# Kernel optimization log

Hardware: AMD Instinct MI355X
Metric: run time of the kernel (lower is better)

The kernel has to match this reference:

```python
import jax, jax.numpy as jnp
import numpy as np

NEG_INF = -9e15  # matches the source's -9000000000000000.0 mask fill
ALPHA = 0.2      # leaky_relu negative slope


def setup_inputs() -> dict:
    key = jax.random.key(0)
    k1, k2, k3, k4 = jax.random.split(key, 4)
    B, N, C_IN, C_OUT, H = 2, 2048, 128, 128, 16
    c = C_OUT // H  # 8 per-head features; equals H//2 so source's a-slice is consistent
    node_feats = jax.random.normal(k1, (B, N, C_IN), dtype=jnp.float32)
    # random 0/1 adjacency with self-loops
    adj = jax.random.randint(k2, (B, N, N), 0, 2).astype(jnp.float32)
    adj = jnp.maximum(adj, jnp.eye(N, dtype=jnp.float32)[None])
    # glorot-uniform-ish params
    W = jax.random.normal(k3, (C_IN, H * c), dtype=jnp.float32) * np.sqrt(2.0 / (C_IN + H * c))
    b = jnp.zeros((H * c,), dtype=jnp.float32)
    a = jax.random.normal(k4, (H, 2 * c), dtype=jnp.float32) * np.sqrt(2.0 / (H + 2 * c))
    return {"node_feats": node_feats, "adj_matrix": adj, "W": W, "b": b, "a": a}


def reference(node_feats, adj_matrix, W, b, a):
    B, N = node_feats.shape[:2]
    H = a.shape[0]
    c = a.shape[1] // 2
    # projection + split into heads: [B, N, H, c]
    h = (node_feats @ W + b).reshape(B, N, H, c)
    # additive attention halves (source slices a along last axis)
    logit_parent = jnp.einsum('bnhc,hc->bnh', h, a[:, :c])
    logit_child = jnp.einsum('bnhc,hc->bnh', h, a[:, c:])
    # dense broadcast-add logits: [B, N(i), N(j), H]
    attn_logits = logit_parent[:, :, None, :] + logit_child[:, None, :, :]
    attn_logits = jax.nn.leaky_relu(attn_logits, negative_slope=ALPHA)
    attn_logits = jnp.where(adj_matrix[..., None] == 1.0, attn_logits, NEG_INF)
    attn_probs = jax.nn.softmax(attn_logits, axis=2)  # over source nodes j
    out = jnp.einsum('bijh,bjhc->bihc', attn_probs, h)
    out = out.reshape(B, N, H * c)  # concat_heads=True
    return out, adj_matrix
```

## Files before the change

kernel.cpp:

```cpp
#include <hip/hip_runtime.h>
#include <hip/hip_bf16.h>


#define B_   2
#define N_   2048
#define CIN_ 128
#define H_   16

typedef _Float16 h2  __attribute__((ext_vector_type(2)));
typedef _Float16 v8h __attribute__((ext_vector_type(8)));
typedef float    v4f __attribute__((ext_vector_type(4)));

#define SC6 0.015625f

__device__ inline h2 pk_f16(float a, float b) {
  return __builtin_bit_cast(h2, __builtin_amdgcn_cvt_pkrtz(a, b));
}
__device__ inline unsigned as_u32(h2 v) { return __builtin_bit_cast(unsigned, v); }
__device__ inline h2 as_h2(unsigned u) { return __builtin_bit_cast(h2, u); }

__global__ __launch_bounds__(128) void proj_kernel(
    const float* __restrict__ nf, const float* __restrict__ W,
    const float* __restrict__ bias, const float* __restrict__ a,
    unsigned* __restrict__ hQ, unsigned* __restrict__ qI,
    float* __restrict__ lpT, unsigned* __restrict__ ones) {
  const int row0 = blockIdx.x * 4;
  const int t    = threadIdx.x;
  if (blockIdx.x == 0) {
    ones[t] = 0x3C003C00u; ones[t + 128] = 0x3C003C00u;
    ones[t + 256] = 0x3C003C00u; ones[t + 384] = 0x3C003C00u;
  }
  __shared__ float sNf[4][CIN_];
  ((float4*)&sNf[0][0])[t] = ((const float4*)(nf + (long)row0 * CIN_))[t];
  __syncthreads();
  float acc[4];
  const float bv = bias[t];
#pragma unroll
  for (int r = 0; r < 4; ++r) acc[r] = bv;
#pragma unroll 8
  for (int k = 0; k < CIN_; ++k) {
    const float w = W[k * 128 + t];
#pragma unroll
    for (int r = 0; r < 4; ++r) acc[r] = fmaf(sNf[r][k], w, acc[r]);
  }
  const int h = t >> 3, kc = t & 7;
  const int b = row0 >> 11, n0 = row0 & (N_ - 1);
  const int bh = b * H_ + h;
  const int cdw = n0 >> 1;
  uint2 hv;
  hv.x = as_u32(pk_f16(acc[0], acc[1]));
  hv.y = as_u32(pk_f16(acc[2], acc[3]));
  *(uint2*)(hQ + ((long)(bh * 8 + kc)) * (N_ / 2) + cdw) = hv;

  const float ap = a[h * 16 + kc], ac = a[h * 16 + 8 + kc];
  float lpv[4], lcv[4];
#pragma unroll
  for (int r = 0; r < 4; ++r) {
    float x = acc[r] * ap, y = acc[r] * ac;
#pragma unroll
    for (int s = 1; s < 8; s <<= 1) {
      x += __shfl_xor(x, s);
      y += __shfl_xor(y, s);
    }
    lpv[r] = x; lcv[r] = y;
  }
  if (kc == 0) {
    float4 l0 = {lpv[0], lpv[1], lpv[2], lpv[3]};
    *(float4*)(lpT + (long)bh * N_ + n0) = l0;
    uint2 q1, q2;
    q1.x = as_u32(pk_f16(__expf(lcv[0]) * SC6, __expf(lcv[1]) * SC6));
    q1.y = as_u32(pk_f16(__expf(lcv[2]) * SC6, __expf(lcv[3]) * SC6));
    q2.x = as_u32(pk_f16(__expf(0.2f * lcv[0]) * SC6, __expf(0.2f * lcv[1]) * SC6));
    q2.y = as_u32(pk_f16(__expf(0.2f * lcv[2]) * SC6, __expf(0.2f * lcv[3]) * SC6));
    const int addr = bh * 2048 + (cdw >> 4) * 32 + ((cdw >> 2) & 3) * 8;
    const int off  = cdw & 3;
    *(uint2*)(qI + addr + off)     = q1;
    *(uint2*)(qI + addr + 4 + off) = q2;
  }
}

__global__ __launch_bounds__(512) void attn_kernel(
    const float* __restrict__ adj, const unsigned* __restrict__ hQ,
    const unsigned* __restrict__ qI, const float* __restrict__ lpT,
    const unsigned* __restrict__ ones, float* __restrict__ pA,
    float* __restrict__ pL, float* __restrict__ adj_out) {
  const int jq   = blockIdx.x & 3;
  const int rest = blockIdx.x >> 2;
  const int b    = rest >> 6;
  const int i0   = (rest & 63) * 32;
  const int tid  = threadIdx.x;
  const int w    = tid >> 6;
  const int lane = tid & 63;

  __shared__ uint4 sA[2048];

  {
    const long aoff = (long)(b * N_ + i0) * N_ + jq * 512;
    const float* abase = adj + aoff;
    float* obase = adj_out + aoff;
    float4 fa[4], fb[4];
    int rowv[4], ccv[4];
#pragma unroll
    for (int s = 0; s < 4; ++s) {
      const int D = s * 512 + tid;
      const int u = D >> 10, loc = D & 1023;
      const int mm = loc & 15, qc = loc >> 4;
      ccv[s] = (qc >> 2) * 32 + (qc & 3) * 8;
      rowv[s] = u * 16 + mm;
      fa[s] = *(const float4*)(abase + (long)rowv[s] * N_ + ccv[s]);
      fb[s] = *(const float4*)(abase + (long)rowv[s] * N_ + ccv[s] + 4);
    }
#pragma unroll
    for (int s = 0; s < 4; ++s) {
      const int D = s * 512 + tid;
      uint4 uu;
      uu.x = as_u32(pk_f16(fa[s].x, fa[s].y)); uu.y = as_u32(pk_f16(fa[s].z, fa[s].w));
      uu.z = as_u32(pk_f16(fb[s].x, fb[s].y)); uu.w = as_u32(pk_f16(fb[s].z, fb[s].w));
      sA[D] = uu;
      *(float4*)(obase + (long)rowv[s] * N_ + ccv[s])     = fa[s];
      *(float4*)(obase + (long)rowv[s] * N_ + ccv[s] + 4) = fb[s];
    }
  }
  __syncthreads();

  const int m  = lane & 15;
  const int q  = lane >> 4;
  const int bh0 = b * H_ + w;
  const int bh1 = bh0 + 8;

  const float lpa0 = lpT[(long)bh0 * N_ + i0 + m];
  const float lpb0 = lpT[(long)bh0 * N_ + i0 + 16 + m];
  const float lpa1 = lpT[(long)bh1 * N_ + i0 + m];
  const float lpb1 = lpT[(long)bh1 * N_ + i0 + 16 + m];
  const h2 P1a0 = pk_f16(__expf(lpa0) * SC6, __expf(lpa0) * SC6);
  const h2 P2a0 = pk_f16(__expf(0.2f * lpa0) * SC6, __expf(0.2f * lpa0) * SC6);
  const h2 P1b0 = pk_f16(__expf(lpb0) * SC6, __expf(lpb0) * SC6);
  const h2 P2b0 = pk_f16(__expf(0.2f * lpb0) * SC6, __expf(0.2f * lpb0) * SC6);
  const h2 P1a1 = pk_f16(__expf(lpa1) * SC6, __expf(lpa1) * SC6);
  const h2 P2a1 = pk_f16(__expf(0.2f * lpa1) * SC6, __expf(0.2f * lpa1) * SC6);
  const h2 P1b1 = pk_f16(__expf(lpb1) * SC6, __expf(lpb1) * SC6);
  const h2 P2b1 = pk_f16(__expf(0.2f * lpb1) * SC6, __expf(0.2f * lpb1) * SC6);

  const unsigned* qp0 = qI + bh0 * 2048 + jq * 512 + q * 8;
  const unsigned* qp1 = qI + bh1 * 2048 + jq * 512 + q * 8;
  const unsigned* hp0 = (m < 8)
      ? hQ + ((long)(bh0 * 8 + m)) * (N_ / 2) + jq * 256 + q * 4
      : ones + q * 4;
  const unsigned* hp1 = (m < 8)
      ? hQ + ((long)(bh1 * 8 + m)) * (N_ / 2) + jq * 256 + q * 4
      : ones + q * 4;

  v4f acc0a = {0.f, 0.f, 0.f, 0.f}, acc1a = {0.f, 0.f, 0.f, 0.f};
  v4f acc0b = {0.f, 0.f, 0.f, 0.f}, acc1b = {0.f, 0.f, 0.f, 0.f};

  uint4 q1X0 = *(const uint4*)(qp0),      q2X0 = *(const uint4*)(qp0 + 4),
        hX0  = *(const uint4*)(hp0);
  uint4 q1X1 = *(const uint4*)(qp1),      q2X1 = *(const uint4*)(qp1 + 4),
        hX1  = *(const uint4*)(hp1);
  uint4 q1Y0 = *(const uint4*)(qp0 + 32), q2Y0 = *(const uint4*)(qp0 + 36),
        hY0  = *(const uint4*)(hp0 + 16);
  uint4 q1Y1 = *(const uint4*)(qp1 + 32), q2Y1 = *(const uint4*)(qp1 + 36),
        hY1  = *(const uint4*)(hp1 + 16);

  for (int t2 = 0; t2 < 8; ++t2) {
    const int ch0 = 2 * t2, ch1 = 2 * t2 + 1;
    const int pq0 = ((ch0 + 2) & 15) * 32, ph0 = ((ch0 + 2) & 15) * 16;
    const int pq1 = ((ch1 + 2) & 15) * 32, ph1 = ((ch1 + 2) & 15) * 16;

    const uint4 n10 = *(const uint4*)(qp0 + pq0);
    const uint4 n20 = *(const uint4*)(qp0 + pq0 + 4);
    const uint4 nh0 = *(const uint4*)(hp0 + ph0);
    const uint4 n11 = *(const uint4*)(qp1 + pq0);
    const uint4 n21 = *(const uint4*)(qp1 + pq0 + 4);
    const uint4 nh1 = *(const uint4*)(hp1 + ph0);
    {
      const uint4 Av0 = sA[ch0 * 64 + lane];
      const uint4 Av1 = sA[1024 + ch0 * 64 + lane];
      {
        const h2 Q1x = as_h2(q1X0.x), Q1y = as_h2(q1X0.y), Q1z = as_h2(q1X0.z), Q1w = as_h2(q1X0.w);
        const h2 Q2x = as_h2(q2X0.x), Q2y = as_h2(q2X0.y), Q2z = as_h2(q2X0.z), Q2w = as_h2(q2X0.w);
        const v8h bf = __builtin_bit_cast(v8h, hX0);
        const uint4 af0 = {
          as_u32(__builtin_elementwise_max(P1a0 * Q1x, P2a0 * Q2x) * as_h2(Av0.x)),
          as_u32(__builtin_elementwise_max(P1a0 * Q1y, P2a0 * Q2y) * as_h2(Av0.y)),
          as_u32(__builtin_elementwise_max(P1a0 * Q1z, P2a0 * Q2z) * as_h2(Av0.z)),
          as_u32(__builtin_elementwise_max(P1a0 * Q1w, P2a0 * Q2w) * as_h2(Av0.w))};
        acc0a = __builtin_amdgcn_mfma_f32_16x16x32_f16(
            __builtin_bit_cast(v8h, af0), bf, acc0a, 0, 0, 0);
        const uint4 af1 = {
          as_u32(__builtin_elementwise_max(P1b0 * Q1x, P2b0 * Q2x) * as_h2(Av1.x)),
          as_u32(__builtin_elementwise_max(P1b0 * Q1y, P2b0 * Q2y) * as_h2(Av1.y)),
          as_u32(__builtin_elementwise_max(P1b0 * Q1z, P2b0 * Q2z) * as_h2(Av1.z)),
          as_u32(__builtin_elementwise_max(P1b0 * Q1w, P2b0 * Q2w) * as_h2(Av1.w))};
        acc1a = __builtin_amdgcn_mfma_f32_16x16x32_f16(
            __builtin_bit_cast(v8h, af1), bf, acc1a, 0, 0, 0);
      }
      {
        const h2 Q1x = as_h2(q1X1.x), Q1y = as_h2(q1X1.y), Q1z = as_h2(q1X1.z), Q1w = as_h2(q1X1.w);
        const h2 Q2x = as_h2(q2X1.x), Q2y = as_h2(q2X1.y), Q2z = as_h2(q2X1.z), Q2w = as_h2(q2X1.w);
        const v8h bf = __builtin_bit_cast(v8h, hX1);
        const uint4 af0 = {
          as_u32(__builtin_elementwise_max(P1a1 * Q1x, P2a1 * Q2x) * as_h2(Av0.x)),
          as_u32(__builtin_elementwise_max(P1a1 * Q1y, P2a1 * Q2y) * as_h2(Av0.y)),
          as_u32(__builtin_elementwise_max(P1a1 * Q1z, P2a1 * Q2z) * as_h2(Av0.z)),
          as_u32(__builtin_elementwise_max(P1a1 * Q1w, P2a1 * Q2w) * as_h2(Av0.w))};
        acc0b = __builtin_amdgcn_mfma_f32_16x16x32_f16(
            __builtin_bit_cast(v8h, af0), bf, acc0b, 0, 0, 0);
        const uint4 af1 = {
          as_u32(__builtin_elementwise_max(P1b1 * Q1x, P2b1 * Q2x) * as_h2(Av1.x)),
          as_u32(__builtin_elementwise_max(P1b1 * Q1y, P2b1 * Q2y) * as_h2(Av1.y)),
          as_u32(__builtin_elementwise_max(P1b1 * Q1z, P2b1 * Q2z) * as_h2(Av1.z)),
          as_u32(__builtin_elementwise_max(P1b1 * Q1w, P2b1 * Q2w) * as_h2(Av1.w))};
        acc1b = __builtin_amdgcn_mfma_f32_16x16x32_f16(
            __builtin_bit_cast(v8h, af1), bf, acc1b, 0, 0, 0);
      }
    }
    q1X0 = n10; q2X0 = n20; hX0 = nh0;
    q1X1 = n11; q2X1 = n21; hX1 = nh1;

    const uint4 m10 = *(const uint4*)(qp0 + pq1);
    const uint4 m20 = *(const uint4*)(qp0 + pq1 + 4);
    const uint4 mh0 = *(const uint4*)(hp0 + ph1);
    const uint4 m11 = *(const uint4*)(qp1 + pq1);
    const uint4 m21 = *(const uint4*)(qp1 + pq1 + 4);
    const uint4 mh1 = *(const uint4*)(hp1 + ph1);
    {
      const uint4 Av0 = sA[ch1 * 64 + lane];
      const uint4 Av1 = sA[1024 + ch1 * 64 + lane];
      {
        const h2 Q1x = as_h2(q1Y0.x), Q1y = as_h2(q1Y0.y), Q1z = as_h2(q1Y0.z), Q1w = as_h2(q1Y0.w);
        const h2 Q2x = as_h2(q2Y0.x), Q2y = as_h2(q2Y0.y), Q2z = as_h2(q2Y0.z), Q2w = as_h2(q2Y0.w);
        const v8h bf = __builtin_bit_cast(v8h, hY0);
        const uint4 af0 = {
          as_u32(__builtin_elementwise_max(P1a0 * Q1x, P2a0 * Q2x) * as_h2(Av0.x)),
          as_u32(__builtin_elementwise_max(P1a0 * Q1y, P2a0 * Q2y) * as_h2(Av0.y)),
          as_u32(__builtin_elementwise_max(P1a0 * Q1z, P2a0 * Q2z) * as_h2(Av0.z)),
          as_u32(__builtin_elementwise_max(P1a0 * Q1w, P2a0 * Q2w) * as_h2(Av0.w))};
        acc0a = __builtin_amdgcn_mfma_f32_16x16x32_f16(
            __builtin_bit_cast(v8h, af0), bf, acc0a, 0, 0, 0);
        const uint4 af1 = {
          as_u32(__builtin_elementwise_max(P1b0 * Q1x, P2b0 * Q2x) * as_h2(Av1.x)),
          as_u32(__builtin_elementwise_max(P1b0 * Q1y, P2b0 * Q2y) * as_h2(Av1.y)),
          as_u32(__builtin_elementwise_max(P1b0 * Q1z, P2b0 * Q2z) * as_h2(Av1.z)),
          as_u32(__builtin_elementwise_max(P1b0 * Q1w, P2b0 * Q2w) * as_h2(Av1.w))};
        acc1a = __builtin_amdgcn_mfma_f32_16x16x32_f16(
            __builtin_bit_cast(v8h, af1), bf, acc1a, 0, 0, 0);
      }
      {
        const h2 Q1x = as_h2(q1Y1.x), Q1y = as_h2(q1Y1.y), Q1z = as_h2(q1Y1.z), Q1w = as_h2(q1Y1.w);
        const h2 Q2x = as_h2(q2Y1.x), Q2y = as_h2(q2Y1.y), Q2z = as_h2(q2Y1.z), Q2w = as_h2(q2Y1.w);
        const v8h bf = __builtin_bit_cast(v8h, hY1);
        const uint4 af0 = {
          as_u32(__builtin_elementwise_max(P1a1 * Q1x, P2a1 * Q2x) * as_h2(Av0.x)),
          as_u32(__builtin_elementwise_max(P1a1 * Q1y, P2a1 * Q2y) * as_h2(Av0.y)),
          as_u32(__builtin_elementwise_max(P1a1 * Q1z, P2a1 * Q2z) * as_h2(Av0.z)),
          as_u32(__builtin_elementwise_max(P1a1 * Q1w, P2a1 * Q2w) * as_h2(Av0.w))};
        acc0b = __builtin_amdgcn_mfma_f32_16x16x32_f16(
            __builtin_bit_cast(v8h, af0), bf, acc0b, 0, 0, 0);
        const uint4 af1 = {
          as_u32(__builtin_elementwise_max(P1b1 * Q1x, P2b1 * Q2x) * as_h2(Av1.x)),
          as_u32(__builtin_elementwise_max(P1b1 * Q1y, P2b1 * Q2y) * as_h2(Av1.y)),
          as_u32(__builtin_elementwise_max(P1b1 * Q1z, P2b1 * Q2z) * as_h2(Av1.z)),
          as_u32(__builtin_elementwise_max(P1b1 * Q1w, P2b1 * Q2w) * as_h2(Av1.w))};
        acc1b = __builtin_amdgcn_mfma_f32_16x16x32_f16(
            __builtin_bit_cast(v8h, af1), bf, acc1b, 0, 0, 0);
      }
    }
    q1Y0 = m10; q2Y0 = m20; hY0 = mh0;
    q1Y1 = m11; q2Y1 = m21; hY1 = mh1;
  }

#pragma unroll
  for (int g = 0; g < 2; ++g) {
    const int hw = g * 8 + w;
#pragma unroll
    for (int u = 0; u < 2; ++u) {
      const v4f av = g ? (u ? acc1b : acc0b) : (u ? acc1a : acc0a);
#pragma unroll
      for (int r = 0; r < 4; ++r) {
        const int gidx = (b * N_ + i0 + u * 16 + q * 4 + r) * H_ + hw;
        if (m < 8)  pA[jq * 524288 + (long)gidx * 8 + m] = av[r];
        if (m == 8) pL[jq * 65536 + gidx] = av[r];
      }
    }
  }
}

__global__ __launch_bounds__(512) void combine_kernel(
    const float* __restrict__ pA, const float* __restrict__ pL,
    float* __restrict__ out) {
  const int g = blockIdx.x * 512 + threadIdx.x;
  const int gl = g >> 3;
  const float s = pL[gl] + pL[gl + 65536] + pL[gl + 131072] + pL[gl + 196608];
  const float v = pA[g] + pA[g + 524288] + pA[g + 1048576] + pA[g + 1572864];
  out[g] = v / s;
}

extern "C" void kernel_launch(void* const* d_in, const int* in_sizes, int n_in,
                              void* d_out, int out_size, void* d_ws, size_t ws_size,
                              hipStream_t stream) {
  const float* nf   = (const float*)d_in[0];
  const float* adj  = (const float*)d_in[1];
  const float* W    = (const float*)d_in[2];
  const float* bias = (const float*)d_in[3];
  const float* a    = (const float*)d_in[4];

  float* out     = (float*)d_out;
  float* adj_out = out + (long)B_ * N_ * H_ * 8;

  unsigned* ws   = (unsigned*)d_ws;
  unsigned* hQ   = ws;
  unsigned* qI   = ws + 262144;
  float*    lpT  = (float*)(ws + 327680);
  unsigned* ones = ws + 393216;
  float*    pA   = (float*)(ws + 393728);
  float*    pL   = (float*)(ws + 2490880);

  hipLaunchKernelGGL(proj_kernel, dim3(B_ * N_ / 4), dim3(128), 0, stream,
                     nf, W, bias, a, hQ, qI, lpT, ones);
  hipLaunchKernelGGL(attn_kernel, dim3(B_ * (N_ / 32) * 4), dim3(512), 0,
                     stream, adj, hQ, qI, lpT, ones, pA, pL, adj_out);
  hipLaunchKernelGGL(combine_kernel, dim3(1024), dim3(512), 0, stream,
                     pA, pL, out);
}
```

Baseline: 131.1 us.

## Stage per-head child-logit tiles in shared memory and deepen h prefetch

At block start, the 16 heads' qI slices for this j-quarter are copied from global memory into a new shared buffer, sQ (32 KB), so the inner loop reads Q values from LDS instead of issuing global loads. The h (B-operand) loads now use a four-deep register ring prefetched four chunks ahead, replacing the two-deep X/Y double buffer. This cuts global load traffic and latency in the MFMA loop. In exchange it raises LDS usage (which may limit occupancy), adds a staging phase, and holds more h registers live.

```diff
diff --git a/kernel.cpp b/kernel.cpp
--- a/kernel.cpp
+++ b/kernel.cpp
@@ -92,8 +92,16 @@
   const int w    = tid >> 6;
   const int lane = tid & 63;
 
-  __shared__ uint4 sA[2048];
-
+  __shared__ uint4    sA[2048];
+  __shared__ unsigned sQ[8192];
+
+  {
+    const int head = tid >> 5;
+    const int off  = (tid & 31) * 16;
+    const uint4* src = (const uint4*)(qI + (b * H_ + head) * 2048 + jq * 512 + off);
+    uint4* dst = (uint4*)(sQ + head * 512 + off);
+    dst[0] = src[0]; dst[1] = src[1]; dst[2] = src[2]; dst[3] = src[3];
+  }
   {
     const long aoff = (long)(b * N_ + i0) * N_ + jq * 512;
     const float* abase = adj + aoff;
@@ -141,8 +149,8 @@
   const h2 P1b1 = pk_f16(__expf(lpb1) * SC6, __expf(lpb1) * SC6);
   const h2 P2b1 = pk_f16(__expf(0.2f * lpb1) * SC6, __expf(0.2f * lpb1) * SC6);
 
-  const unsigned* qp0 = qI + bh0 * 2048 + jq * 512 + q * 8;
-  const unsigned* qp1 = qI + bh1 * 2048 + jq * 512 + q * 8;
+  const unsigned* sq0 = sQ + w * 512 + q * 8;
+  const unsigned* sq1 = sQ + (w + 8) * 512 + q * 8;
   const unsigned* hp0 = (m < 8)
       ? hQ + ((long)(bh0 * 8 + m)) * (N_ / 2) + jq * 256 + q * 4
       : ones + q * 4;
@@ -153,33 +161,32 @@
   v4f acc0a = {0.f, 0.f, 0.f, 0.f}, acc1a = {0.f, 0.f, 0.f, 0.f};
   v4f acc0b = {0.f, 0.f, 0.f, 0.f}, acc1b = {0.f, 0.f, 0.f, 0.f};
 
-  uint4 q1X0 = *(const uint4*)(qp0),      q2X0 = *(const uint4*)(qp0 + 4),
-        hX0  = *(const uint4*)(hp0);
-  uint4 q1X1 = *(const uint4*)(qp1),      q2X1 = *(const uint4*)(qp1 + 4),
-        hX1  = *(const uint4*)(hp1);
-  uint4 q1Y0 = *(const uint4*)(qp0 + 32), q2Y0 = *(const uint4*)(qp0 + 36),
-        hY0  = *(const uint4*)(hp0 + 16);
-  uint4 q1Y1 = *(const uint4*)(qp1 + 32), q2Y1 = *(const uint4*)(qp1 + 36),
-        hY1  = *(const uint4*)(hp1 + 16);
-
-  for (int t2 = 0; t2 < 8; ++t2) {
-    const int ch0 = 2 * t2, ch1 = 2 * t2 + 1;
-    const int pq0 = ((ch0 + 2) & 15) * 32, ph0 = ((ch0 + 2) & 15) * 16;
-    const int pq1 = ((ch1 + 2) & 15) * 32, ph1 = ((ch1 + 2) & 15) * 16;
-
-    const uint4 n10 = *(const uint4*)(qp0 + pq0);
-    const uint4 n20 = *(const uint4*)(qp0 + pq0 + 4);
-    const uint4 nh0 = *(const uint4*)(hp0 + ph0);
-    const uint4 n11 = *(const uint4*)(qp1 + pq0);
-    const uint4 n21 = *(const uint4*)(qp1 + pq0 + 4);
-    const uint4 nh1 = *(const uint4*)(hp1 + ph0);
-    {
-      const uint4 Av0 = sA[ch0 * 64 + lane];
-      const uint4 Av1 = sA[1024 + ch0 * 64 + lane];
+  uint4 h0[4], h1[4];
+#pragma unroll
+  for (int d = 0; d < 4; ++d) {
+    h0[d] = *(const uint4*)(hp0 + d * 16);
+    h1[d] = *(const uint4*)(hp1 + d * 16);
+  }
+
+  for (int t4 = 0; t4 < 4; ++t4) {
+#pragma unroll
+    for (int s = 0; s < 4; ++s) {
+      const int ch = t4 * 4 + s;
+      const int pf = ((ch + 4) & 15) * 16;
+      const uint4 n0 = *(const uint4*)(hp0 + pf);
+      const uint4 n1 = *(const uint4*)(hp1 + pf);
+
+      const uint4 q1c0 = *(const uint4*)(sq0 + ch * 32);
+      const uint4 q2c0 = *(const uint4*)(sq0 + ch * 32 + 4);
+      const uint4 q1c1 = *(const uint4*)(sq1 + ch * 32);
+      const uint4 q2c1 = *(const uint4*)(sq1 + ch * 32 + 4);
+      const uint4 Av0 = sA[ch * 64 + lane];
+      const uint4 Av1 = sA[1024 + ch * 64 + lane];
+
       {
-        const h2 Q1x = as_h2(q1X0.x), Q1y = as_h2(q1X0.y), Q1z = as_h2(q1X0.z), Q1w = as_h2(q1X0.w);
-        const h2 Q2x = as_h2(q2X0.x), Q2y = as_h2(q2X0.y), Q2z = as_h2(q2X0.z), Q2w = as_h2(q2X0.w);
-        const v8h bf = __builtin_bit_cast(v8h, hX0);
+        const h2 Q1x = as_h2(q1c0.x), Q1y = as_h2(q1c0.y), Q1z = as_h2(q1c0.z), Q1w = as_h2(q1c0.w);
+        const h2 Q2x = as_h2(q2c0.x), Q2y = as_h2(q2c0.y), Q2z = as_h2(q2c0.z), Q2w = as_h2(q2c0.w);
+        const v8h bf = __builtin_bit_cast(v8h, h0[s]);
         const uint4 af0 = {
           as_u32(__builtin_elementwise_max(P1a0 * Q1x, P2a0 * Q2x) * as_h2(Av0.x)),
           as_u32(__builtin_elementwise_max(P1a0 * Q1y, P2a0 * Q2y) * as_h2(Av0.y)),
@@ -196,9 +203,9 @@
             __builtin_bit_cast(v8h, af1), bf, acc1a, 0, 0, 0);
       }
       {
-        const h2 Q1x = as_h2(q1X1.x), Q1y = as_h2(q1X1.y), Q1z = as_h2(q1X1.z), Q1w = as_h2(q1X1.w);
-        const h2 Q2x = as_h2(q2X1.x), Q2y = as_h2(q2X1.y), Q2z = as_h2(q2X1.z), Q2w = as_h2(q2X1.w);
-        const v8h bf = __builtin_bit_cast(v8h, hX1);
+        const h2 Q1x = as_h2(q1c1.x), Q1y = as_h2(q1c1.y), Q1z = as_h2(q1c1.z), Q1w = as_h2(q1c1.w);
+        const h2 Q2x = as_h2(q2c1.x), Q2y = as_h2(q2c1.y), Q2z = as_h2(q2c1.z), Q2w = as_h2(q2c1.w);
+        const v8h bf = __builtin_bit_cast(v8h, h1[s]);
         const uint4 af0 = {
           as_u32(__builtin_elementwise_max(P1a1 * Q1x, P2a1 * Q2x) * as_h2(Av0.x)),
           as_u32(__builtin_elementwise_max(P1a1 * Q1y, P2a1 * Q2y) * as_h2(Av0.y)),
@@ -214,60 +221,8 @@
         acc1b = __builtin_amdgcn_mfma_f32_16x16x32_f16(
             __builtin_bit_cast(v8h, af1), bf, acc1b, 0, 0, 0);
       }
-    }
-    q1X0 = n10; q2X0 = n20; hX0 = nh0;
-    q1X1 = n11; q2X1 = n21; hX1 = nh1;
-
-    const uint4 m10 = *(const uint4*)(qp0 + pq1);
-    const uint4 m20 = *(const uint4*)(qp0 + pq1 + 4);
-    const uint4 mh0 = *(const uint4*)(hp0 + ph1);
-    const uint4 m11 = *(const uint4*)(qp1 + pq1);
-    const uint4 m21 = *(const uint4*)(qp1 + pq1 + 4);
-    const uint4 mh1 = *(const uint4*)(hp1 + ph1);
-    {
-      const uint4 Av0 = sA[ch1 * 64 + lane];
-      const uint4 Av1 = sA[1024 + ch1 * 64 + lane];
-      {
-        const h2 Q1x = as_h2(q1Y0.x), Q1y = as_h2(q1Y0.y), Q1z = as_h2(q1Y0.z), Q1w = as_h2(q1Y0.w);
-        const h2 Q2x = as_h2(q2Y0.x), Q2y = as_h2(q2Y0.y), Q2z = as_h2(q2Y0.z), Q2w = as_h2(q2Y0.w);
-        const v8h bf = __builtin_bit_cast(v8h, hY0);
-        const uint4 af0 = {
-          as_u32(__builtin_elementwise_max(P1a0 * Q1x, P2a0 * Q2x) * as_h2(Av0.x)),
-          as_u32(__builtin_elementwise_max(P1a0 * Q1y, P2a0 * Q2y) * as_h2(Av0.y)),
-          as_u32(__builtin_elementwise_max(P1a0 * Q1z, P2a0 * Q2z) * as_h2(Av0.z)),
-          as_u32(__builtin_elementwise_max(P1a0 * Q1w, P2a0 * Q2w) * as_h2(Av0.w))};
-        acc0a = __builtin_amdgcn_mfma_f32_16x16x32_f16(
-            __builtin_bit_cast(v8h, af0), bf, acc0a, 0, 0, 0);
-        const uint4 af1 = {
-          as_u32(__builtin_elementwise_max(P1b0 * Q1x, P2b0 * Q2x) * as_h2(Av1.x)),
-          as_u32(__builtin_elementwise_max(P1b0 * Q1y, P2b0 * Q2y) * as_h2(Av1.y)),
-          as_u32(__builtin_elementwise_max(P1b0 * Q1z, P2b0 * Q2z) * as_h2(Av1.z)),
-          as_u32(__builtin_elementwise_max(P1b0 * Q1w, P2b0 * Q2w) * as_h2(Av1.w))};
-        acc1a = __builtin_amdgcn_mfma_f32_16x16x32_f16(
-            __builtin_bit_cast(v8h, af1), bf, acc1a, 0, 0, 0);
-      }
-      {
-        const h2 Q1x = as_h2(q1Y1.x), Q1y = as_h2(q1Y1.y), Q1z = as_h2(q1Y1.z), Q1w = as_h2(q1Y1.w);
-        const h2 Q2x = as_h2(q2Y1.x), Q2y = as_h2(q2Y1.y), Q2z = as_h2(q2Y1.z), Q2w = as_h2(q2Y1.w);
-        const v8h bf = __builtin_bit_cast(v8h, hY1);
-        const uint4 af0 = {
-          as_u32(__builtin_elementwise_max(P1a1 * Q1x, P2a1 * Q2x) * as_h2(Av0.x)),
-          as_u32(__builtin_elementwise_max(P1a1 * Q1y, P2a1 * Q2y) * as_h2(Av0.y)),
-          as_u32(__builtin_elementwise_max(P1a1 * Q1z, P2a1 * Q2z) * as_h2(Av0.z)),
-          as_u32(__builtin_elementwise_max(P1a1 * Q1w, P2a1 * Q2w) * as_h2(Av0.w))};
-        acc0b = __builtin_amdgcn_mfma_f32_16x16x32_f16(
-            __builtin_bit_cast(v8h, af0), bf, acc0b, 0, 0, 0);
-        const uint4 af1 = {
-          as_u32(__builtin_elementwise_max(P1b1 * Q1x, P2b1 * Q2x) * as_h2(Av1.x)),
-          as_u32(__builtin_elementwise_max(P1b1 * Q1y, P2b1 * Q2y) * as_h2(Av1.y)),
-          as_u32(__builtin_elementwise_max(P1b1 * Q1z, P2b1 * Q2z) * as_h2(Av1.z)),
-          as_u32(__builtin_elementwise_max(P1b1 * Q1w, P2b1 * Q2w) * as_h2(Av1.w))};
-        acc1b = __builtin_amdgcn_mfma_f32_16x16x32_f16(
-            __builtin_bit_cast(v8h, af1), bf, acc1b, 0, 0, 0);
-      }
-    }
-    q1Y0 = m10; q2Y0 = m20; hY0 = mh0;
-    q1Y1 = m11; q2Y1 = m21; hY1 = mh1;
+      h0[s] = n0; h1[s] = n1;
+    }
   }
 
 #pragma unroll
```

After: 123.0 us. -6.2%, faster.
